# Optimization experiments

Hardware: AMD Instinct MI355X
Metric: run time of the kernel (lower is better)

The kernel has to match this reference:

```python
import jax, jax.numpy as jnp
import numpy as np

EPS = 1e-5
N0, K1, K2 = 1000, 500, 100  # node counts fixed by the view() calls in the source


def _conv_bn_relu(x, w, b, g, be):
    # Conv1d(k=1) == per-node linear; BatchNorm1d in training mode over nodes
    h = x @ w.T + b                      # (N, Cout)
    mu = h.mean(0)
    var = h.var(0)                       # biased variance, as torch BN uses
    return jax.nn.relu(g * (h - mu) * jax.lax.rsqrt(var + EPS) + be)


def _linear_relu(x, w, b):
    return jax.nn.relu(x @ w.T + b)


def _sag_pool(x, src, dst, ew, w_rel, w_root, bias, k):
    # SAGPooling with GraphConv scorer (sum aggregation weighted by edge_attr)
    N = x.shape[0]
    agg = jax.ops.segment_sum(ew[:, None] * x[src], dst, num_segments=N)  # (N, C)
    score = agg @ w_rel + x @ w_root + bias                               # (N,)
    top_s, perm = jax.lax.top_k(score, k)
    xk = x[perm] * jnp.tanh(top_s)[:, None]                               # (k, C)
    # re-index edges: keep only edges between surviving nodes (mask, fixed E)
    new_idx = jnp.zeros(N, jnp.int32).at[perm].set(jnp.arange(k, dtype=jnp.int32))
    keep = jnp.zeros(N, bool).at[perm].set(True)
    valid = keep[src] & keep[dst]
    nsrc = jnp.where(valid, new_idx[src], 0)
    ndst = jnp.where(valid, new_idx[dst], 0)
    new_ew = jnp.where(valid, ew, 0.0)  # zero weight == edge removed
    return xk, nsrc, ndst, new_ew


def setup_inputs() -> dict:
    key = jax.random.key(0)
    ks = jax.random.split(key, 32)
    nrm = lambda k, sh, s=0.05: jax.random.normal(k, sh, jnp.float32) * s
    E = 32000
    return {
        "x": jax.random.normal(ks[0], (1, N0, 3), jnp.float32),
        "edge_index": jax.random.randint(ks[1], (2, E), 0, N0, jnp.int32),
        "edge_attr": jax.random.uniform(ks[2], (E,), jnp.float32),
        # input: Conv1d(3,64)+BN
        "w0": nrm(ks[3], (64, 3)), "b0": jnp.zeros(64), "g0": jnp.ones(64), "be0": jnp.zeros(64),
        # mlp_first: Conv1d(64,64)+BN
        "w1": nrm(ks[4], (64, 64)), "b1": jnp.zeros(64), "g1": jnp.ones(64), "be1": jnp.zeros(64),
        # mlp_second: Conv1d(64,128)+BN, Conv1d(128,200)+BN
        "w2a": nrm(ks[5], (128, 64)), "b2a": jnp.zeros(128), "g2a": jnp.ones(128), "be2a": jnp.zeros(128),
        "w2b": nrm(ks[6], (200, 128)), "b2b": jnp.zeros(200), "g2b": jnp.ones(200), "be2b": jnp.zeros(200),
        # mlp_third: Conv1d(200,128), Conv1d(128,2) (no BN)
        "w3a": nrm(ks[7], (128, 200)), "b3a": jnp.zeros(128),
        "w3b": nrm(ks[8], (2, 128)), "b3b": jnp.zeros(2),
        # SAGPooling scorers (GraphConv(in_channels, 1))
        "p1_wrel": nrm(ks[9], (64,)), "p1_wroot": nrm(ks[10], (64,)), "p1_b": jnp.zeros(()),
        "p2_wrel": nrm(ks[11], (200,)), "p2_wroot": nrm(ks[12], (200,)), "p2_b": jnp.zeros(()),
    }


def reference(x, edge_index, edge_attr,
              w0, b0, g0, be0, w1, b1, g1, be1,
              w2a, b2a, g2a, be2a, w2b, b2b, g2b, be2b,
              w3a, b3a, w3b, b3b,
              p1_wrel, p1_wroot, p1_b, p2_wrel, p2_wroot, p2_b):
    h = x.reshape(N0, 3)
    src, dst = edge_index[0], edge_index[1]
    ew = edge_attr.reshape(-1)

    h = _conv_bn_relu(h, w0, b0, g0, be0)      # (1000, 64)
    h = _conv_bn_relu(h, w1, b1, g1, be1)      # (1000, 64)
    h, src, dst, ew = _sag_pool(h, src, dst, ew, p1_wrel, p1_wroot, p1_b, K1)

    h = _conv_bn_relu(h, w2a, b2a, g2a, be2a)  # (500, 128)
    h = _conv_bn_relu(h, w2b, b2b, g2b, be2b)  # (500, 200)
    h, src, dst, ew = _sag_pool(h, src, dst, ew, p2_wrel, p2_wroot, p2_b, K2)

    g = h.max(0)                               # global max pool over 100 nodes -> (200,)
    h3 = _linear_relu(g, w3a, b3a)             # (128,)
    out = _linear_relu(h3, w3b, b3b)           # (2,)
    return jax.nn.log_softmax(out)[None, :]    # (1, 2)
```

## Files before the change

### kernel.cpp

```cpp
#include <hip/hip_runtime.h>
#include <math.h>

#define EPS 1e-5f
#define N0 1000
#define NK1 500
#define NK2 100
#define NE 32000

__device__ __forceinline__ float bnr(float h, float sc, float sh) {
    float v = fmaf(h, sc, sh);
    return v > 0.f ? v : 0.f;
}

__global__ __launch_bounds__(256) void k_lin01(
        const float* __restrict__ x, const float* __restrict__ w0,
        const float* __restrict__ b0, const float* __restrict__ g0,
        const float* __restrict__ be0, const float* __restrict__ w1,
        const float* __restrict__ b1, float* __restrict__ h1,
        float* __restrict__ psum1, float* __restrict__ sc1, float* __restrict__ sc2) {
    __shared__ float xs[16][68], wsm[64][65];
    __shared__ float sc0[64], sh0[64];
    __shared__ float redA[256], redB[256];
    __shared__ float mom[4][9];
    const int b = blockIdx.x, t = threadIdx.x;
    const int c = t & 63, slot = t >> 6;
    const int lane = t & 63, wv = t >> 6;
    const int nb = b * 16;

    int gid = b * 256 + t;
    if (gid < 1000) sc1[gid] = 0.f;
    else if (gid < 1500) sc2[gid - 1000] = 0.f;

    {
        float mm[9] = {0.f, 0.f, 0.f, 0.f, 0.f, 0.f, 0.f, 0.f, 0.f};
        for (int n = t; n < N0; n += 256) {
            float x0 = x[3 * n], x1 = x[3 * n + 1], x2 = x[3 * n + 2];
            mm[0] += x0; mm[1] += x1; mm[2] += x2;
            mm[3] += x0 * x0; mm[4] += x1 * x1; mm[5] += x2 * x2;
            mm[6] += x0 * x1; mm[7] += x0 * x2; mm[8] += x1 * x2;
        }
        #pragma unroll
        for (int k = 0; k < 9; ++k) {
            #pragma unroll
            for (int msk = 32; msk >= 1; msk >>= 1) mm[k] += __shfl_xor(mm[k], msk, 64);
        }
        if (lane < 9) mom[wv][lane] = mm[lane] * 0.f;
        if (lane == 0) {
            #pragma unroll
            for (int k = 0; k < 9; ++k) mom[wv][k] = mm[k];
        }
        __syncthreads();
        if (t < 64) {
            float M0 = mom[0][0] + mom[1][0] + mom[2][0] + mom[3][0];
            float M1 = mom[0][1] + mom[1][1] + mom[2][1] + mom[3][1];
            float M2 = mom[0][2] + mom[1][2] + mom[2][2] + mom[3][2];
            float P00 = mom[0][3] + mom[1][3] + mom[2][3] + mom[3][3];
            float P11 = mom[0][4] + mom[1][4] + mom[2][4] + mom[3][4];
            float P22 = mom[0][5] + mom[1][5] + mom[2][5] + mom[3][5];
            float P01 = mom[0][6] + mom[1][6] + mom[2][6] + mom[3][6];
            float P02 = mom[0][7] + mom[1][7] + mom[2][7] + mom[3][7];
            float P12 = mom[0][8] + mom[1][8] + mom[2][8] + mom[3][8];
            float wa = w0[t * 3], wb = w0[t * 3 + 1], wc = w0[t * 3 + 2], bb = b0[t];
            float lin = wa * M0 + wb * M1 + wc * M2;
            float S = lin + (float)N0 * bb;
            float Q = wa * wa * P00 + wb * wb * P11 + wc * wc * P22
                    + 2.f * (wa * wb * P01 + wa * wc * P02 + wb * wc * P12)
                    + 2.f * bb * lin + (float)N0 * bb * bb;
            float mu = S * (1.f / N0);
            float var = Q * (1.f / N0) - mu * mu;
            float sv = g0[t] * rsqrtf(var + EPS);
            sc0[t] = sv; sh0[t] = be0[t] - mu * sv;
        }
        __syncthreads();
    }
    for (int i = 0; i < 4; ++i) {
        int e = t + i * 256;
        int r = e >> 6, cc = e & 63;
        int n = nb + r;
        float v = 0.f;
        if (n < N0) {
            float h = fmaf(w0[cc * 3], x[n * 3],
                      fmaf(w0[cc * 3 + 1], x[n * 3 + 1],
                      fmaf(w0[cc * 3 + 2], x[n * 3 + 2], b0[cc])));
            v = bnr(h, sc0[cc], sh0[cc]);
        }
        xs[r][cc] = v;
    }
    for (int i = 0; i < 16; ++i) {
        int e = t + i * 256;
        wsm[e >> 6][e & 63] = w1[e];
    }
    __syncthreads();
    const int r0 = slot * 4;
    float bb1 = b1[c];
    float a0 = bb1, a1 = bb1, a2 = bb1, a3 = bb1;
    #pragma unroll
    for (int kq = 0; kq < 16; ++kq) {
        float w0v = wsm[c][4 * kq],     w1v = wsm[c][4 * kq + 1];
        float w2v = wsm[c][4 * kq + 2], w3v = wsm[c][4 * kq + 3];
        float4 x0 = *(const float4*)&xs[r0 + 0][4 * kq];
        float4 x1 = *(const float4*)&xs[r0 + 1][4 * kq];
        float4 x2 = *(const float4*)&xs[r0 + 2][4 * kq];
        float4 x3 = *(const float4*)&xs[r0 + 3][4 * kq];
        a0 = fmaf(x0.x, w0v, fmaf(x0.y, w1v, fmaf(x0.z, w2v, fmaf(x0.w, w3v, a0))));
        a1 = fmaf(x1.x, w0v, fmaf(x1.y, w1v, fmaf(x1.z, w2v, fmaf(x1.w, w3v, a1))));
        a2 = fmaf(x2.x, w0v, fmaf(x2.y, w1v, fmaf(x2.z, w2v, fmaf(x2.w, w3v, a2))));
        a3 = fmaf(x3.x, w0v, fmaf(x3.y, w1v, fmaf(x3.z, w2v, fmaf(x3.w, w3v, a3))));
    }
    float av[4] = {a0, a1, a2, a3};
    float sacc = 0.f, qacc = 0.f;
    #pragma unroll
    for (int i = 0; i < 4; ++i) {
        int n = nb + r0 + i;
        if (n < N0) {
            h1[n * 64 + c] = av[i];
            sacc += av[i]; qacc += av[i] * av[i];
        }
    }
    __syncthreads();
    redA[t] = sacc; redB[t] = qacc;
    __syncthreads();
    if (t < 64) {
        psum1[t * 64 + b]        = redA[t] + redA[t + 64] + redA[t + 128] + redA[t + 192];
        psum1[(64 + t) * 64 + b] = redB[t] + redB[t + 64] + redB[t + 128] + redB[t + 192];
    }
}

__device__ __forceinline__ float sum64c(const float* p) {
    const float4* p4 = (const float4*)p;
    float4 a = p4[0];
    #pragma unroll
    for (int i = 1; i < 16; ++i) {
        float4 v = p4[i];
        a.x += v.x; a.y += v.y; a.z += v.z; a.w += v.w;
    }
    return (a.x + a.y) + (a.z + a.w);
}
__device__ __forceinline__ float sum32c(const float* p) {
    const float4* p4 = (const float4*)p;
    float4 a = p4[0];
    #pragma unroll
    for (int i = 1; i < 8; ++i) {
        float4 v = p4[i];
        a.x += v.x; a.y += v.y; a.z += v.z; a.w += v.w;
    }
    return (a.x + a.y) + (a.z + a.w);
}

__global__ __launch_bounds__(256) void k_pool1scat(
        const float* __restrict__ h1, const float* __restrict__ psum1,
        const float* __restrict__ g1, const float* __restrict__ be1,
        const float* __restrict__ wrel, const float* __restrict__ wroot,
        const float* __restrict__ pb, const int* __restrict__ ei,
        const float* __restrict__ ea, float* __restrict__ sc1) {
    __shared__ float tt[1008], rt[1008], acc[1008];
    __shared__ float bsc[64], bsh[64];
    __shared__ float red[128];
    const int b = blockIdx.x, t = threadIdx.x;
    if (t < 128) red[t] = sum64c(psum1 + t * 64);
    for (int i = t; i < 1008; i += 256) acc[i] = 0.f;
    __syncthreads();
    if (t < 64) {
        float mu = red[t] * (1.f / N0);
        float var = red[64 + t] * (1.f / N0) - mu * mu;
        float sv = g1[t] * rsqrtf(var + EPS);
        bsc[t] = sv; bsh[t] = be1[t] - mu * sv;
    }
    __syncthreads();
    {
        const int sub = t & 3, grp = t >> 2;
        float wrv[16], wov[16], scv[16], shv[16];
        #pragma unroll
        for (int i = 0; i < 16; ++i) {
            int ch = sub * 16 + i;
            wrv[i] = wrel[ch]; wov[i] = wroot[ch];
            scv[i] = bsc[ch];  shv[i] = bsh[ch];
        }
        float pbv = pb[0];
        for (int p = 0; p < 16; ++p) {
            int n = p * 64 + grp;
            if (n < N0) {
                const float* hp = h1 + n * 64 + sub * 16;
                float dr = 0.f, dt = 0.f;
                #pragma unroll
                for (int i = 0; i < 16; ++i) {
                    float v = bnr(hp[i], scv[i], shv[i]);
                    dr = fmaf(v, wrv[i], dr);
                    dt = fmaf(v, wov[i], dt);
                }
                dr += __shfl_xor(dr, 1, 64); dr += __shfl_xor(dr, 2, 64);
                dt += __shfl_xor(dt, 1, 64); dt += __shfl_xor(dt, 2, 64);
                if (sub == 0) { tt[n] = dr; rt[n] = dt + pbv; }
            }
        }
    }
    __syncthreads();
    for (int e = b * 2000 + t; e < b * 2000 + 2000; e += 256) {
        float w = ea[e];
        if (w != 0.f) atomicAdd(&acc[ei[NE + e]], w * tt[ei[e]]);
    }
    __syncthreads();
    {
        int n = b * 63 + t;
        if (t < 63 && n < N0) atomicAdd(&sc1[n], rt[n]);
    }
    for (int i = t; i < N0; i += 256) {
        float v = acc[i];
        if (v != 0.f) atomicAdd(&sc1[i], v);
    }
}

__global__ __launch_bounds__(256) void k_rank1_lin2a(
        const float* __restrict__ h1, const float* __restrict__ psum1,
        const float* __restrict__ g1, const float* __restrict__ be1,
        const float* __restrict__ sc1, const float* __restrict__ w2a,
        const float* __restrict__ b2a, float* __restrict__ h2a,
        float* __restrict__ psum2a, int* __restrict__ rk_g) {
    __shared__ float ss[N0];
    __shared__ float xp[16][68];
    __shared__ float wsm[128][65];
    __shared__ float bsc[64], bsh[64];
    __shared__ float red[256], redq[256];
    __shared__ int rloc[16], svj[16];
    __shared__ float thv[16];
    __shared__ int nsS;
    const int b = blockIdx.x, t = threadIdx.x;
    const int lane = t & 63, wv = t >> 6;
    const int nb = b * 16;
    const int nn = (N0 - nb) < 0 ? 0 : ((N0 - nb) < 16 ? (N0 - nb) : 16);

    for (int i = t; i < N0; i += 256) ss[i] = sc1[i];
    if (t < 128) red[t] = sum64c(psum1 + t * 64);
    __syncthreads();
    if (t < 64) {
        float mu = red[t] * (1.f / N0);
        float var = red[64 + t] * (1.f / N0) - mu * mu;
        float sv = g1[t] * rsqrtf(var + EPS);
        bsc[t] = sv; bsh[t] = be1[t] - mu * sv;
    }
    __syncthreads();
    for (int it = 0; it < 4; ++it) {
        int j = it * 4 + wv;
        int n = nb + j;
        if (j < nn) {
            float s = ss[n];
            int r = 0;
            for (int m = lane; m < N0; m += 64) {
                float x = ss[m];
                r += (x > s) || (x == s && m < n);
            }
            #pragma unroll
            for (int msk = 32; msk >= 1; msk >>= 1) r += __shfl_xor(r, msk, 64);
            if (lane == 0) { rk_g[n] = r; rloc[j] = r; }
        } else if (lane == 0) rloc[j] = 1 << 20;
    }
    __syncthreads();
    if (t == 0) {
        int c_ = 0;
        for (int j = 0; j < 16; ++j)
            if (rloc[j] < NK1) { svj[c_] = j; ++c_; }
        nsS = c_;
    }
    __syncthreads();
    const int ns = nsS;
    if (t < ns) thv[t] = tanhf(ss[nb + svj[t]]);
    __syncthreads();
    for (int e = t; e < 16 * 64; e += 256) {
        int i = e >> 6, c = e & 63;
        xp[i][c] = (i < ns) ? bnr(h1[(nb + svj[i]) * 64 + c], bsc[c], bsh[c]) * thv[i] : 0.f;
    }
    for (int e = t; e < 128 * 64; e += 256)
        wsm[e >> 6][e & 63] = w2a[e];
    __syncthreads();
    const int c2 = t & 127, half = t >> 7;
    float hac[8];
    {
        float bb = b2a[c2];
        #pragma unroll
        for (int i = 0; i < 8; ++i) hac[i] = bb;
    }
    #pragma unroll
    for (int kq = 0; kq < 16; ++kq) {
        float w0v = wsm[c2][4 * kq],     w1v = wsm[c2][4 * kq + 1];
        float w2v = wsm[c2][4 * kq + 2], w3v = wsm[c2][4 * kq + 3];
        #pragma unroll
        for (int i = 0; i < 8; ++i) {
            float4 x4 = *(const float4*)&xp[half * 8 + i][4 * kq];
            hac[i] = fmaf(x4.x, w0v, fmaf(x4.y, w1v, fmaf(x4.z, w2v, fmaf(x4.w, w3v, hac[i]))));
        }
    }
    float s = 0.f, q = 0.f;
    #pragma unroll
    for (int i = 0; i < 8; ++i) {
        int sl = half * 8 + i;
        if (sl < ns) {
            int r = rloc[svj[sl]];
            h2a[r * 128 + c2] = hac[i];
            s += hac[i]; q += hac[i] * hac[i];
        }
    }
    __syncthreads();
    red[t] = s; redq[t] = q;
    __syncthreads();
    if (t < 128) {
        psum2a[t * 64 + b]         = red[t] + red[t + 128];
        psum2a[(128 + t) * 64 + b] = redq[t] + redq[t + 128];
    }
}

__global__ __launch_bounds__(256) void k_lin2b(
        const float* __restrict__ h2a, const float* __restrict__ psum2a,
        const float* __restrict__ g2a, const float* __restrict__ be2a,
        const float* __restrict__ w2b, const float* __restrict__ b2b,
        float* __restrict__ h2b, float* __restrict__ psum2b) {
    __shared__ float zL[16][132];
    __shared__ float sc[128], sh[128];
    __shared__ float red[256];
    const int b = blockIdx.x, t = threadIdx.x;
    const int nb = b * 16;
    const int nrows = (NK1 - nb) < 16 ? (NK1 - nb) : 16;
    if (t < 256) red[t] = sum64c(psum2a + t * 64);
    __syncthreads();
    if (t < 128) {
        float mu = red[t] * (1.f / NK1);
        float var = red[128 + t] * (1.f / NK1) - mu * mu;
        float sv = g2a[t] * rsqrtf(var + EPS);
        sc[t] = sv; sh[t] = be2a[t] - mu * sv;
    }
    __syncthreads();
    for (int e = t; e < 16 * 128; e += 256) {
        int r = e >> 7, k = e & 127;
        zL[r][k] = (r < nrows) ? bnr(h2a[(nb + r) * 128 + k], sc[k], sh[k]) : 0.f;
    }
    __syncthreads();
    if (t < 200) {
        float acc[16];
        float bb = b2b[t];
        #pragma unroll
        for (int i = 0; i < 16; ++i) acc[i] = bb;
        for (int kq = 0; kq < 32; ++kq) {
            float4 w4 = *(const float4*)&w2b[t * 128 + 4 * kq];
            #pragma unroll
            for (int i = 0; i < 16; ++i) {
                float4 z4 = *(const float4*)&zL[i][4 * kq];
                acc[i] = fmaf(z4.x, w4.x, fmaf(z4.y, w4.y, fmaf(z4.z, w4.z, fmaf(z4.w, w4.w, acc[i]))));
            }
        }
        float s = 0.f, q = 0.f;
        #pragma unroll
        for (int i = 0; i < 16; ++i) {
            if (i < nrows) {
                h2b[(nb + i) * 200 + t] = acc[i];
                s += acc[i]; q += acc[i] * acc[i];
            }
        }
        psum2b[t * 32 + b]         = s;
        psum2b[(200 + t) * 32 + b] = q;
    }
}

__global__ __launch_bounds__(256) void k_pool2scat(
        const float* __restrict__ h2b, const float* __restrict__ psum2b,
        const float* __restrict__ g2b, const float* __restrict__ be2b,
        const float* __restrict__ wrel, const float* __restrict__ wroot,
        const float* __restrict__ pb, const int* __restrict__ ei,
        const float* __restrict__ ea, const int* __restrict__ rk_g,
        float* __restrict__ sc2) {
    __shared__ float tt[512], rt[512], acc[512], tmp[400];
    __shared__ float bsc[200], bsh[200];
    const int b = blockIdx.x, t = threadIdx.x;
    for (int idx = t; idx < 400; idx += 256) tmp[idx] = sum32c(psum2b + idx * 32);
    for (int i = t; i < 512; i += 256) acc[i] = 0.f;
    __syncthreads();
    if (t < 200) {
        float mu = tmp[t] * (1.f / NK1);
        float var = tmp[200 + t] * (1.f / NK1) - mu * mu;
        float sv = g2b[t] * rsqrtf(var + EPS);
        bsc[t] = sv; bsh[t] = be2b[t] - mu * sv;
    }
    __syncthreads();
    {
        const int sub = t & 3, grp = t >> 2;
        float pbv = pb[0];
        for (int p = 0; p < 8; ++p) {
            int n = p * 64 + grp;
            if (n < NK1) {
                const float* hp = h2b + n * 200 + sub * 50;
                float dr = 0.f, dt = 0.f;
                for (int i = 0; i < 50; ++i) {
                    int ch = sub * 50 + i;
                    float v = bnr(hp[i], bsc[ch], bsh[ch]);
                    dr = fmaf(v, wrel[ch], dr);
                    dt = fmaf(v, wroot[ch], dt);
                }
                dr += __shfl_xor(dr, 1, 64); dr += __shfl_xor(dr, 2, 64);
                dt += __shfl_xor(dt, 1, 64); dt += __shfl_xor(dt, 2, 64);
                if (sub == 0) { tt[n] = dr; rt[n] = dt + pbv; }
            }
        }
    }
    __syncthreads();
    for (int e = b * 2000 + t; e < b * 2000 + 2000; e += 256) {
        float w = ea[e];
        if (w != 0.f) {
            int rs = rk_g[ei[e]], rd = rk_g[ei[NE + e]];
            if (rs < NK1 && rd < NK1) atomicAdd(&acc[rd], w * tt[rs]);
        }
    }
    __syncthreads();
    {
        int n = b * 32 + t;
        if (t < 32 && n < NK1) atomicAdd(&sc2[n], rt[n]);
    }
    for (int i = t; i < NK1; i += 256) {
        float v = acc[i];
        if (v != 0.f) atomicAdd(&sc2[i], v);
    }
}

__global__ __launch_bounds__(1024) void k_final(
        const float* __restrict__ h2b, const float* __restrict__ psum2b,
        const float* __restrict__ g2b, const float* __restrict__ be2b,
        const float* __restrict__ sc2, const float* __restrict__ w3a,
        const float* __restrict__ b3a, const float* __restrict__ w3b,
        const float* __restrict__ b3b, float* __restrict__ out) {
    __shared__ float ss[512], tmp[400];
    __shared__ float bsc[200], bsh[200];
    __shared__ int pn[NK2];
    __shared__ float th[NK2];
    __shared__ float gp[16 * 200];
    __shared__ float g[200], h3[128], o[2];
    const int t = threadIdx.x;
    const int lane = t & 63, wv = t >> 6;

    for (int idx = t; idx < 400; idx += 1024) tmp[idx] = sum32c(psum2b + idx * 32);
    for (int i = t; i < NK1; i += 1024) ss[i] = sc2[i];
    for (int i = t; i < 16 * 200; i += 1024) gp[i] = -1e30f;
    __syncthreads();
    if (t < 200) {
        float mu = tmp[t] * (1.f / NK1);
        float var = tmp[200 + t] * (1.f / NK1) - mu * mu;
        float sv = g2b[t] * rsqrtf(var + EPS);
        bsc[t] = sv; bsh[t] = be2b[t] - mu * sv;
    }
    __syncthreads();
    for (int n = wv; n < NK1; n += 16) {
        float s = ss[n];
        int r = 0;
        for (int m = lane; m < NK1; m += 64) {
            float x = ss[m];
            r += (x > s) || (x == s && m < n);
        }
        #pragma unroll
        for (int msk = 32; msk >= 1; msk >>= 1) r += __shfl_xor(r, msk, 64);
        if (lane == 0 && r < NK2) { pn[r] = n; th[r] = tanhf(s); }
    }
    __syncthreads();
    for (int j = wv; j < NK2; j += 16) {
        int n = pn[j];
        float tn = th[j];
        #pragma unroll
        for (int jj = 0; jj < 4; ++jj) {
            int ch = lane + 64 * jj;
            if (ch < 200) {
                float v = bnr(h2b[n * 200 + ch], bsc[ch], bsh[ch]) * tn;
                gp[wv * 200 + ch] = fmaxf(gp[wv * 200 + ch], v);
            }
        }
    }
    __syncthreads();
    if (t < 200) {
        float m = gp[t];
        #pragma unroll
        for (int i = 1; i < 16; ++i) m = fmaxf(m, gp[i * 200 + t]);
        g[t] = m;
    }
    __syncthreads();
    for (int r = wv; r < 128; r += 16) {
        float p = 0.f;
        #pragma unroll
        for (int jj = 0; jj < 4; ++jj) {
            int ch = lane + 64 * jj;
            if (ch < 200) p = fmaf(w3a[r * 200 + ch], g[ch], p);
        }
        #pragma unroll
        for (int m = 32; m >= 1; m >>= 1) p += __shfl_xor(p, m, 64);
        if (lane == 0) h3[r] = fmaxf(p + b3a[r], 0.f);
    }
    __syncthreads();
    if (t < 128) {
        int ow = t >> 6;
        float p = w3b[ow * 128 + lane] * h3[lane]
                + w3b[ow * 128 + 64 + lane] * h3[64 + lane];
        #pragma unroll
        for (int m = 32; m >= 1; m >>= 1) p += __shfl_xor(p, m, 64);
        if (lane == 0) o[ow] = fmaxf(p + b3b[ow], 0.f);
    }
    __syncthreads();
    if (t == 0) {
        float m = fmaxf(o[0], o[1]);
        float l = m + logf(expf(o[0] - m) + expf(o[1] - m));
        out[0] = o[0] - l;
        out[1] = o[1] - l;
    }
}

extern "C" void kernel_launch(void* const* d_in, const int* in_sizes, int n_in,
                              void* d_out, int out_size, void* d_ws, size_t ws_size,
                              hipStream_t stream) {
    const float* x    = (const float*)d_in[0];
    const int*   ei   = (const int*)d_in[1];
    const float* ea   = (const float*)d_in[2];
    const float* w0   = (const float*)d_in[3];
    const float* b0   = (const float*)d_in[4];
    const float* g0   = (const float*)d_in[5];
    const float* be0  = (const float*)d_in[6];
    const float* w1   = (const float*)d_in[7];
    const float* b1   = (const float*)d_in[8];
    const float* g1   = (const float*)d_in[9];
    const float* be1  = (const float*)d_in[10];
    const float* w2a  = (const float*)d_in[11];
    const float* b2a  = (const float*)d_in[12];
    const float* g2a  = (const float*)d_in[13];
    const float* be2a = (const float*)d_in[14];
    const float* w2b  = (const float*)d_in[15];
    const float* b2b  = (const float*)d_in[16];
    const float* g2b  = (const float*)d_in[17];
    const float* be2b = (const float*)d_in[18];
    const float* w3a  = (const float*)d_in[19];
    const float* b3a  = (const float*)d_in[20];
    const float* w3b  = (const float*)d_in[21];
    const float* b3b  = (const float*)d_in[22];
    const float* p1_wrel  = (const float*)d_in[23];
    const float* p1_wroot = (const float*)d_in[24];
    const float* p1_b     = (const float*)d_in[25];
    const float* p2_wrel  = (const float*)d_in[26];
    const float* p2_wroot = (const float*)d_in[27];
    const float* p2_b     = (const float*)d_in[28];

    float* ws = (float*)d_ws;
    float* h1     = ws;
    float* h2a    = ws + 64000;
    float* h2b    = ws + 128000;
    float* psum1  = ws + 228000;
    float* psum2a = ws + 236192;
    float* psum2b = ws + 252576;
    float* sc1    = ws + 265376;
    float* sc2    = ws + 266376;
    int*   rk_g   = (int*)(ws + 266876);
    float* out    = (float*)d_out;

    k_lin01<<<64, 256, 0, stream>>>(x, w0, b0, g0, be0, w1, b1, h1, psum1, sc1, sc2);
    k_pool1scat<<<16, 256, 0, stream>>>(h1, psum1, g1, be1, p1_wrel, p1_wroot, p1_b,
                                        ei, ea, sc1);
    k_rank1_lin2a<<<64, 256, 0, stream>>>(h1, psum1, g1, be1, sc1, w2a, b2a,
                                          h2a, psum2a, rk_g);
    k_lin2b<<<32, 256, 0, stream>>>(h2a, psum2a, g2a, be2a, w2b, b2b, h2b, psum2b);
    k_pool2scat<<<16, 256, 0, stream>>>(h2b, psum2b, g2b, be2b, p2_wrel, p2_wroot, p2_b,
                                        ei, ea, rk_g, sc2);
    k_final<<<1, 1024, 0, stream>>>(h2b, psum2b, g2b, be2b, sc2, w3a, b3a, w3b, b3b, out);
}
```

Baseline: 111.1 us.

## Fuse second pooling scatter into single-block final kernel; read w2a directly

Merges the 16-block k_pool2scat into the single 1024-thread k_final. The second-pool scores are now computed in shared memory (root term plus an edge scatter over all 32000 edges), which removes the global sc2 buffer, its zeroing, the global atomics and one kernel launch. It also drops the shared-memory staging of w2a in k_rank1_lin2a in favour of direct float4 global loads. The trade-off is that one workgroup now processes every edge serially instead of 16 blocks sharing the work.

```diff
diff --git a/kernel.cpp b/kernel.cpp
--- a/kernel.cpp
+++ b/kernel.cpp
@@ -17,7 +17,7 @@
         const float* __restrict__ b0, const float* __restrict__ g0,
         const float* __restrict__ be0, const float* __restrict__ w1,
         const float* __restrict__ b1, float* __restrict__ h1,
-        float* __restrict__ psum1, float* __restrict__ sc1, float* __restrict__ sc2) {
+        float* __restrict__ psum1, float* __restrict__ sc1) {
     __shared__ float xs[16][68], wsm[64][65];
     __shared__ float sc0[64], sh0[64];
     __shared__ float redA[256], redB[256];
@@ -29,7 +29,6 @@
 
     int gid = b * 256 + t;
     if (gid < 1000) sc1[gid] = 0.f;
-    else if (gid < 1500) sc2[gid - 1000] = 0.f;
 
     {
         float mm[9] = {0.f, 0.f, 0.f, 0.f, 0.f, 0.f, 0.f, 0.f, 0.f};
@@ -44,7 +43,6 @@
             #pragma unroll
             for (int msk = 32; msk >= 1; msk >>= 1) mm[k] += __shfl_xor(mm[k], msk, 64);
         }
-        if (lane < 9) mom[wv][lane] = mm[lane] * 0.f;
         if (lane == 0) {
             #pragma unroll
             for (int k = 0; k < 9; ++k) mom[wv][k] = mm[k];
@@ -218,7 +216,6 @@
         float* __restrict__ psum2a, int* __restrict__ rk_g) {
     __shared__ float ss[N0];
     __shared__ float xp[16][68];
-    __shared__ float wsm[128][65];
     __shared__ float bsc[64], bsh[64];
     __shared__ float red[256], redq[256];
     __shared__ int rloc[16], svj[16];
@@ -269,8 +266,6 @@
         int i = e >> 6, c = e & 63;
         xp[i][c] = (i < ns) ? bnr(h1[(nb + svj[i]) * 64 + c], bsc[c], bsh[c]) * thv[i] : 0.f;
     }
-    for (int e = t; e < 128 * 64; e += 256)
-        wsm[e >> 6][e & 63] = w2a[e];
     __syncthreads();
     const int c2 = t & 127, half = t >> 7;
     float hac[8];
@@ -281,12 +276,11 @@
     }
     #pragma unroll
     for (int kq = 0; kq < 16; ++kq) {
-        float w0v = wsm[c2][4 * kq],     w1v = wsm[c2][4 * kq + 1];
-        float w2v = wsm[c2][4 * kq + 2], w3v = wsm[c2][4 * kq + 3];
+        float4 w4 = *(const float4*)&w2a[c2 * 64 + 4 * kq];
         #pragma unroll
         for (int i = 0; i < 8; ++i) {
             float4 x4 = *(const float4*)&xp[half * 8 + i][4 * kq];
-            hac[i] = fmaf(x4.x, w0v, fmaf(x4.y, w1v, fmaf(x4.z, w2v, fmaf(x4.w, w3v, hac[i]))));
+            hac[i] = fmaf(x4.x, w4.x, fmaf(x4.y, w4.y, fmaf(x4.z, w4.z, fmaf(x4.w, w4.w, hac[i]))));
         }
     }
     float s = 0.f, q = 0.f;
@@ -359,18 +353,27 @@
     }
 }
 
-__global__ __launch_bounds__(256) void k_pool2scat(
+__global__ __launch_bounds__(1024) void k_final(
         const float* __restrict__ h2b, const float* __restrict__ psum2b,
         const float* __restrict__ g2b, const float* __restrict__ be2b,
         const float* __restrict__ wrel, const float* __restrict__ wroot,
         const float* __restrict__ pb, const int* __restrict__ ei,
         const float* __restrict__ ea, const int* __restrict__ rk_g,
-        float* __restrict__ sc2) {
-    __shared__ float tt[512], rt[512], acc[512], tmp[400];
+        const float* __restrict__ w3a, const float* __restrict__ b3a,
+        const float* __restrict__ w3b, const float* __restrict__ b3b,
+        float* __restrict__ out) {
+    __shared__ float tt[512], rt[512], accs[512], ss[512], tmp[400];
     __shared__ float bsc[200], bsh[200];
-    const int b = blockIdx.x, t = threadIdx.x;
-    for (int idx = t; idx < 400; idx += 256) tmp[idx] = sum32c(psum2b + idx * 32);
-    for (int i = t; i < 512; i += 256) acc[i] = 0.f;
+    __shared__ int pn[NK2];
+    __shared__ float th[NK2];
+    __shared__ float gp[16 * 200];
+    __shared__ float g[200], h3[128], o[2];
+    const int t = threadIdx.x;
+    const int lane = t & 63, wv = t >> 6;
+
+    for (int idx = t; idx < 400; idx += 1024) tmp[idx] = sum32c(psum2b + idx * 32);
+    if (t < 512) accs[t] = 0.f;
+    for (int i = t; i < 16 * 200; i += 1024) gp[i] = -1e30f;
     __syncthreads();
     if (t < 200) {
         float mu = tmp[t] * (1.f / NK1);
@@ -382,8 +385,9 @@
     {
         const int sub = t & 3, grp = t >> 2;
         float pbv = pb[0];
-        for (int p = 0; p < 8; ++p) {
-            int n = p * 64 + grp;
+        #pragma unroll
+        for (int p = 0; p < 2; ++p) {
+            int n = p * 256 + grp;
             if (n < NK1) {
                 const float* hp = h2b + n * 200 + sub * 50;
                 float dr = 0.f, dt = 0.f;
@@ -400,49 +404,15 @@
         }
     }
     __syncthreads();
-    for (int e = b * 2000 + t; e < b * 2000 + 2000; e += 256) {
+    for (int e = t; e < NE; e += 1024) {
         float w = ea[e];
         if (w != 0.f) {
             int rs = rk_g[ei[e]], rd = rk_g[ei[NE + e]];
-            if (rs < NK1 && rd < NK1) atomicAdd(&acc[rd], w * tt[rs]);
-        }
-    }
-    __syncthreads();
-    {
-        int n = b * 32 + t;
-        if (t < 32 && n < NK1) atomicAdd(&sc2[n], rt[n]);
-    }
-    for (int i = t; i < NK1; i += 256) {
-        float v = acc[i];
-        if (v != 0.f) atomicAdd(&sc2[i], v);
-    }
-}
-
-__global__ __launch_bounds__(1024) void k_final(
-        const float* __restrict__ h2b, const float* __restrict__ psum2b,
-        const float* __restrict__ g2b, const float* __restrict__ be2b,
-        const float* __restrict__ sc2, const float* __restrict__ w3a,
-        const float* __restrict__ b3a, const float* __restrict__ w3b,
-        const float* __restrict__ b3b, float* __restrict__ out) {
-    __shared__ float ss[512], tmp[400];
-    __shared__ float bsc[200], bsh[200];
-    __shared__ int pn[NK2];
-    __shared__ float th[NK2];
-    __shared__ float gp[16 * 200];
-    __shared__ float g[200], h3[128], o[2];
-    const int t = threadIdx.x;
-    const int lane = t & 63, wv = t >> 6;
-
-    for (int idx = t; idx < 400; idx += 1024) tmp[idx] = sum32c(psum2b + idx * 32);
-    for (int i = t; i < NK1; i += 1024) ss[i] = sc2[i];
-    for (int i = t; i < 16 * 200; i += 1024) gp[i] = -1e30f;
-    __syncthreads();
-    if (t < 200) {
-        float mu = tmp[t] * (1.f / NK1);
-        float var = tmp[200 + t] * (1.f / NK1) - mu * mu;
-        float sv = g2b[t] * rsqrtf(var + EPS);
-        bsc[t] = sv; bsh[t] = be2b[t] - mu * sv;
-    }
+            if (rs < NK1 && rd < NK1) atomicAdd(&accs[rd], w * tt[rs]);
+        }
+    }
+    __syncthreads();
+    for (int i = t; i < NK1; i += 1024) ss[i] = rt[i] + accs[i];
     __syncthreads();
     for (int n = wv; n < NK1; n += 16) {
         float s = ss[n];
@@ -546,17 +516,15 @@
     float* psum2a = ws + 236192;
     float* psum2b = ws + 252576;
     float* sc1    = ws + 265376;
-    float* sc2    = ws + 266376;
-    int*   rk_g   = (int*)(ws + 266876);
+    int*   rk_g   = (int*)(ws + 266376);
     float* out    = (float*)d_out;
 
-    k_lin01<<<64, 256, 0, stream>>>(x, w0, b0, g0, be0, w1, b1, h1, psum1, sc1, sc2);
+    k_lin01<<<64, 256, 0, stream>>>(x, w0, b0, g0, be0, w1, b1, h1, psum1, sc1);
     k_pool1scat<<<16, 256, 0, stream>>>(h1, psum1, g1, be1, p1_wrel, p1_wroot, p1_b,
                                         ei, ea, sc1);
     k_rank1_lin2a<<<64, 256, 0, stream>>>(h1, psum1, g1, be1, sc1, w2a, b2a,
                                           h2a, psum2a, rk_g);
     k_lin2b<<<32, 256, 0, stream>>>(h2a, psum2a, g2a, be2a, w2b, b2b, h2b, psum2b);
-    k_pool2scat<<<16, 256, 0, stream>>>(h2b, psum2b, g2b, be2b, p2_wrel, p2_wroot, p2_b,
-                                        ei, ea, rk_g, sc2);
-    k_final<<<1, 1024, 0, stream>>>(h2b, psum2b, g2b, be2b, sc2, w3a, b3a, w3b, b3b, out);
-}
+    k_final<<<1, 1024, 0, stream>>>(h2b, psum2b, g2b, be2b, p2_wrel, p2_wroot, p2_b,
+                                    ei, ea, rk_g, w3a, b3a, w3b, b3b, out);
+}
```

Result: slower. 123.5 us (+11.1%).
